# Kernel tuning notes

Hardware: AMD Instinct MI355X
Metric: run time of the kernel (lower is better)

Reference implementation:

```python
import jax, jax.numpy as jnp
import numpy as np

N_NODES = 20000
IN_CH = 128
OUT_CH = 128
HEADS = 1
OB_DIM = 4
N_STEP = 32           # = HEADS*OUT_CH*8 // 32
D_PE = 16             # 32 - HEADS*16
N_EDGES = 256000


def setup_inputs() -> dict:
    key = jax.random.key(0)
    ks = jax.random.split(key, 9)
    x = jax.random.normal(ks[0], (N_NODES, IN_CH), jnp.float32)
    p_t = jax.random.normal(ks[1], (N_STEP, D_PE), jnp.float32)
    edge_index = jax.random.randint(ks[2], (2, N_EDGES), 0, N_NODES, jnp.int32)
    edge_weights = jax.random.uniform(ks[3], (N_EDGES,), jnp.float32)
    # Linear params (PyTorch default init: U(-1/sqrt(fan_in), 1/sqrt(fan_in)))
    s = 1.0 / np.sqrt(IN_CH)
    lin_value_w = jax.random.uniform(ks[4], (IN_CH, HEADS * OUT_CH), jnp.float32, -s, s)
    lin_value_b = jax.random.uniform(ks[5], (HEADS * OUT_CH,), jnp.float32, -s, s)
    inc_w = jax.random.uniform(ks[6], (IN_CH, HEADS * OUT_CH * 8), jnp.float32, -s, s)
    inc_b = jax.random.uniform(ks[7], (HEADS * OUT_CH * 8,), jnp.float32, -s, s)
    g = np.sqrt(6.0 / (N_NODES + HEADS * 16))  # glorot
    map_weights = jax.random.uniform(ks[8], (N_NODES, HEADS * 16), jnp.float32, -g, g)
    return {"x": x, "p_t": p_t, "edge_index": edge_index, "edge_weights": edge_weights,
            "lin_value_w": lin_value_w, "lin_value_b": lin_value_b,
            "inc_w": inc_w, "inc_b": inc_b, "map_weights": map_weights}


def _segment_softmax(gamma, index, num_segments):
    # PyG-style softmax over edges grouped by destination index, per column
    m = jax.ops.segment_max(gamma, index, num_segments=num_segments)     # [N, D]
    num = jnp.exp(gamma - m[index])
    den = jax.ops.segment_sum(num, index, num_segments=num_segments)    # [N, D]
    return num / den[index]


def reference(x, p_t, edge_index, edge_weights, lin_value_w, lin_value_b,
              inc_w, inc_b, map_weights):
    src = edge_index[0]   # x_j side
    dst = edge_index[1]   # x_i side (flow source_to_target)
    n_step = p_t.shape[0]
    E = src.shape[0]

    x_i = x[dst]                                             # [E, in]
    # h_W = increase_dim(x_i).view(E, n_step, 32)
    h_W = (x_i @ inc_w + inc_b).reshape(E, n_step, 32)       # [E, T, 32]
    w_v = map_weights[dst]                                   # [E, 16]
    # beta = mean(h_W * cat([w_v, p_t], -1), -1) computed without materializing aa
    beta = (jnp.einsum('etk,ek->et', h_W[:, :, :16], w_v)
            + jnp.einsum('etk,tk->et', h_W[:, :, 16:], p_t)) / 32.0   # [E, T]

    gamma = beta * edge_weights[:, None]                     # [E, T]
    gamma = jnp.repeat(gamma, OB_DIM, axis=-1)               # [E, T*ob_dim] = [E, H*out]
    all_edge_weights = jnp.mean(gamma, axis=1)               # [E]

    K = int(E * 0.5)
    _, top_idx = jax.lax.top_k(all_edge_weights, K)          # top-K edges
    gamma = gamma[top_idx]                                   # [K, H*out]
    x_i = x_i[top_idx]                                       # [K, in]
    # NOTE: the module re-points aggregation index to edge_index[0] (source)
    index = src[top_idx]                                     # [K]

    gamma = _segment_softmax(gamma, index, N_NODES)          # [K, H*out]

    v = jax.nn.relu(x_i @ lin_value_w + lin_value_b)         # [K, H*out]
    msg = (v.reshape(K, HEADS, OUT_CH)
           * gamma.reshape(K, HEADS, OUT_CH))                # [K, H, out]

    out = jax.ops.segment_sum(msg.reshape(K, HEADS * OUT_CH), index,
                              num_segments=N_NODES)          # scatter-add
    return out                                               # [N, H*out]
```

## Files before the change

kernel.cpp:

```cpp
#include <hip/hip_runtime.h>

#define NN 20000
#define IC 128
#define OC 128
#define NSTEP 32
#define NE 256000
#define KSEL 128000
#define NB 79
#define CH 64
#define ECH 4000
#define RND 16
#define HPW 10000
#define CANDCAP 65536
#define NQCOL 704

struct SelState {
  unsigned long long prefix;
  unsigned r;
  unsigned selc;
  unsigned tiec;
  unsigned done[8];
};

typedef __attribute__((ext_vector_type(16))) float f16v;

__global__ void k_init(const float* __restrict__ p_t, const float* __restrict__ lin_w,
                       const float* __restrict__ lin_b,
                       const float* __restrict__ inc_w, const float* __restrict__ inc_b,
                       float* __restrict__ Wq,
                       double* __restrict__ Ud, double* __restrict__ ubd,
                       unsigned* __restrict__ hist, SelState* st) {
  int i = blockIdx.x * blockDim.x + threadIdx.x;
  if (i < 33 * NQCOL) {
    int k4 = i / NQCOL, col = i - k4 * NQCOL;
    float4 o;
    float* ov = (float*)&o;
    for (int jj = 0; jj < 4; ++jj) {
      int k = 4 * k4 + jj;
      float v = 0.f;
      if (col < 512) {
        int t = col >> 4, c = col & 15;
        if (k < 128) v = inc_w[k * 1024 + t * 32 + c];
        else if (k == 128) v = inc_b[t * 32 + c];
      } else if (col < 544) {
        int t = col - 512;
        if (k < 128) {
          float a = 0.f;
          for (int q = 0; q < 16; ++q) a += inc_w[k * 1024 + t * 32 + 16 + q] * p_t[t * 16 + q];
          v = a;
        } else if (k == 128) {
          float a = 0.f;
          for (int q = 0; q < 16; ++q) a += inc_b[t * 32 + 16 + q] * p_t[t * 16 + q];
          v = a;
        }
      } else if (col < 672) {
        int c = col - 544;
        if (k < 128) v = lin_w[k * OC + c];
        else if (k == 128) v = lin_b[c];
      }
      ov[jj] = v;
    }
    ((float4*)Wq)[i] = o;
    return;
  }
  i -= 33 * NQCOL;
  if (i < 17 * IC) {
    int c = i >> 7, k = i & 127;
    double a = 0.0;
    if (c < 16) {
      for (int t = 0; t < NSTEP; ++t) a += (double)inc_w[k * 1024 + t * 32 + c];
    } else {
      for (int t = 0; t < NSTEP; ++t)
        for (int q = 0; q < 16; ++q)
          a += (double)inc_w[k * 1024 + t * 32 + 16 + q] * (double)p_t[t * 16 + q];
    }
    Ud[c * IC + k] = a;
    return;
  }
  i -= 17 * IC;
  if (i < 17) {
    double a = 0.0;
    if (i < 16) {
      for (int t = 0; t < NSTEP; ++t) a += (double)inc_b[t * 32 + i];
    } else {
      for (int t = 0; t < NSTEP; ++t)
        for (int q = 0; q < 16; ++q)
          a += (double)inc_b[t * 32 + 16 + q] * (double)p_t[t * 16 + q];
    }
    ubd[i] = a;
    return;
  }
  i -= 17;
  if (i < 512) { hist[i] = 0u; return; }
  i -= 512;
  if (i == 0) {
    st->prefix = 0ull; st->r = KSEL; st->selc = 0u; st->tiec = 0u;
    for (int p = 0; p < 8; ++p) st->done[p] = 0u;
  }
}

#define FMA4(WV, BASE)                                                                        \
  acc[BASE+0] = fmaf(xf.x, WV[0],  fmaf(xf.y, WV[1],  fmaf(xf.z, WV[2],  fmaf(xf.w, WV[3],  acc[BASE+0])))); \
  acc[BASE+1] = fmaf(xf.x, WV[4],  fmaf(xf.y, WV[5],  fmaf(xf.z, WV[6],  fmaf(xf.w, WV[7],  acc[BASE+1])))); \
  acc[BASE+2] = fmaf(xf.x, WV[8],  fmaf(xf.y, WV[9],  fmaf(xf.z, WV[10], fmaf(xf.w, WV[11], acc[BASE+2])))); \
  acc[BASE+3] = fmaf(xf.x, WV[12], fmaf(xf.y, WV[13], fmaf(xf.z, WV[14], fmaf(xf.w, WV[15], acc[BASE+3]))));

__global__ __launch_bounds__(256) void k_node(
    const float* __restrict__ x, const float* __restrict__ mw,
    const float* __restrict__ Wq,
    float* __restrict__ beta, float* __restrict__ V) {
  __shared__ float4 xl[64 * 32];
  int tid = threadIdx.x;
  int g = blockIdx.x;
  int s = blockIdx.y;
  int n0 = g * 64;
  int nvalid = NN - n0; if (nvalid > 64) nvalid = 64;

  for (int i = tid; i < 64 * 32; i += 256) {
    int mm = i >> 5, k4 = i & 31;
    float4 v = make_float4(0.f, 0.f, 0.f, 0.f);
    if (mm < nvalid) v = ((const float4*)(x + (size_t)(n0 + mm) * IC))[k4];
    xl[(mm << 5) + ((k4 + mm) & 31)] = v;
  }
  int m = tid & 63;
  int j = __builtin_amdgcn_readfirstlane(threadIdx.x >> 6);
  __syncthreads();

  for (int r = 0; r < 2; ++r) {
    int u = s * 8 + j + r * 4;
    if (u < 32) {
      float mwr[16];
      {
        int mm = (m < nvalid) ? m : 0;
        const float4* mp = (const float4*)(mw + (size_t)(n0 + mm) * 16);
#pragma unroll
        for (int i = 0; i < 4; ++i) {
          float4 t4 = mp[i];
          mwr[4 * i] = t4.x; mwr[4 * i + 1] = t4.y; mwr[4 * i + 2] = t4.z; mwr[4 * i + 3] = t4.w;
        }
      }
      const f16v*   wb = (const f16v*)Wq + (u << 2);
      const float4* wp = (const float4*)Wq + (512 + u);
      float acc[16], accp;
      {
        const f16v* wkb = wb + 32 * 176;
        f16v b0 = wkb[0], b1 = wkb[1], b2 = wkb[2], b3 = wkb[3];
#pragma unroll
        for (int c = 0; c < 4; ++c) {
          acc[c] = b0[4 * c]; acc[4 + c] = b1[4 * c];
          acc[8 + c] = b2[4 * c]; acc[12 + c] = b3[4 * c];
        }
        accp = wp[32 * NQCOL].x;
      }
      f16v w0 = wb[0], w1 = wb[1], w2 = wb[2], w3 = wb[3];
      float4 pw = wp[0];
      for (int k4 = 0; k4 < 32; ++k4) {
        f16v nw0, nw1, nw2, nw3; float4 npw;
        if (k4 < 31) {
          const f16v* wn = wb + (k4 + 1) * 176;
          nw0 = wn[0]; nw1 = wn[1]; nw2 = wn[2]; nw3 = wn[3];
          npw = wp[(k4 + 1) * NQCOL];
        }
        float4 xf = xl[(m << 5) + ((k4 + m) & 31)];
        FMA4(w0, 0) FMA4(w1, 4) FMA4(w2, 8) FMA4(w3, 12)
        accp = fmaf(xf.x, pw.x, fmaf(xf.y, pw.y, fmaf(xf.z, pw.z, fmaf(xf.w, pw.w, accp))));
        if (k4 < 31) { w0 = nw0; w1 = nw1; w2 = nw2; w3 = nw3; pw = npw; }
      }
      float bs = accp;
#pragma unroll
      for (int c = 0; c < 16; ++c) bs = fmaf(acc[c], mwr[c], bs);
      if (m < nvalid) beta[(size_t)(n0 + m) * NSTEP + u] = bs * (1.f / 32.f);
    } else {
      int vg = u - 32;
      int vc0 = vg << 4;
      const f16v* wb = (const f16v*)Wq + 136 + (vg << 2);
      float acc[16];
      {
        const f16v* wkb = wb + 32 * 176;
        f16v b0 = wkb[0], b1 = wkb[1], b2 = wkb[2], b3 = wkb[3];
#pragma unroll
        for (int c = 0; c < 4; ++c) {
          acc[c] = b0[4 * c]; acc[4 + c] = b1[4 * c];
          acc[8 + c] = b2[4 * c]; acc[12 + c] = b3[4 * c];
        }
      }
      f16v w0 = wb[0], w1 = wb[1], w2 = wb[2], w3 = wb[3];
      for (int k4 = 0; k4 < 32; ++k4) {
        f16v nw0, nw1, nw2, nw3;
        if (k4 < 31) {
          const f16v* wn = wb + (k4 + 1) * 176;
          nw0 = wn[0]; nw1 = wn[1]; nw2 = wn[2]; nw3 = wn[3];
        }
        float4 xf = xl[(m << 5) + ((k4 + m) & 31)];
        FMA4(w0, 0) FMA4(w1, 4) FMA4(w2, 8) FMA4(w3, 12)
        if (k4 < 31) { w0 = nw0; w1 = nw1; w2 = nw2; w3 = nw3; }
      }
      if (m < nvalid) {
        float* vout = V + (size_t)(n0 + m) * OC + vc0;
#pragma unroll
        for (int q = 0; q < 4; ++q) {
          float4 o;
          o.x = fmaxf(acc[4 * q], 0.f);     o.y = fmaxf(acc[4 * q + 1], 0.f);
          o.z = fmaxf(acc[4 * q + 2], 0.f); o.w = fmaxf(acc[4 * q + 3], 0.f);
          ((float4*)vout)[q] = o;
        }
      }
    }
  }
}

__global__ __launch_bounds__(256) void k_s64(
    const float* __restrict__ x, const float* __restrict__ mw,
    const double* __restrict__ Ud, const double* __restrict__ ubd,
    double* __restrict__ s64) {
  __shared__ double udl[17 * 130];
  __shared__ float4 xs[16 * 32];
  int tid = threadIdx.x;
  for (int i = tid; i < 17 * IC; i += 256) {
    int cc = i >> 7, kk = i & 127;
    udl[cc * 130 + kk] = Ud[i];
  }
  int n0 = blockIdx.x * 16;
  for (int i = tid; i < 16 * 32; i += 256) {
    int mm = i >> 5, k4 = i & 31;
    int n = n0 + mm;
    xs[i] = (n < NN) ? ((const float4*)(x + (size_t)n * IC))[k4]
                     : make_float4(0.f, 0.f, 0.f, 0.f);
  }
  __syncthreads();
  int m = tid >> 4, c = tid & 15;
  int n = n0 + m;
  const double* uc  = udl + c * 130;
  const double* u16 = udl + 16 * 130;
  double a = 0.0, a16 = 0.0;
  for (int k4 = 0; k4 < 32; ++k4) {
    float4 xv = xs[(m << 5) + k4];
    a = fma((double)xv.x, uc[4 * k4],     a);
    a = fma((double)xv.y, uc[4 * k4 + 1], a);
    a = fma((double)xv.z, uc[4 * k4 + 2], a);
    a = fma((double)xv.w, uc[4 * k4 + 3], a);
  }
#pragma unroll
  for (int q = 0; q < 2; ++q) {
    int k4 = 2 * c + q;
    float4 xv = xs[(m << 5) + k4];
    a16 = fma((double)xv.x, u16[4 * k4],     a16);
    a16 = fma((double)xv.y, u16[4 * k4 + 1], a16);
    a16 = fma((double)xv.z, u16[4 * k4 + 2], a16);
    a16 = fma((double)xv.w, u16[4 * k4 + 3], a16);
  }
  int nm = (n < NN) ? n : 0;
  double part = (a + ubd[c]) * (double)mw[(size_t)nm * 16 + c] + a16;
#pragma unroll
  for (int d = 1; d < 16; d <<= 1) part += __shfl_xor(part, d, 64);
  if (c == 0 && n < NN) s64[n] = (part + ubd[16]) * (1.0 / 1024.0);
}

__global__ void k_keysel(const int* __restrict__ ei, const float* __restrict__ ew,
                         const double* __restrict__ s64,
                         unsigned long long* __restrict__ keys,
                         unsigned* __restrict__ hist, SelState* st) {
  __shared__ unsigned h[256], suf[256];
  __shared__ int last;
  int tid = threadIdx.x;
  h[tid] = 0u;
  if (tid == 0) last = 0;
  __syncthreads();
  for (int e = blockIdx.x * 256 + tid; e < NE; e += gridDim.x * 256) {
    int d = ei[NE + e];
    double v = s64[d] * (double)ew[e];
    unsigned long long u = (unsigned long long)__double_as_longlong(v);
    u = (u & 0x8000000000000000ull) ? ~u : (u | 0x8000000000000000ull);
    keys[e] = u;
    atomicAdd(&h[(unsigned)(u >> 56)], 1u);
  }
  __syncthreads();
  if (h[tid]) atomicAdd(&hist[tid], h[tid]);
  __threadfence();
  __syncthreads();
  if (tid == 0) {
    if (atomicAdd(&st->done[0], 1u) == gridDim.x - 1) last = 1;
  }
  __syncthreads();
  if (!last) return;
  unsigned c = atomicAdd(&hist[tid], 0u);
  suf[tid] = c;
  __syncthreads();
  for (int d = 1; d < 256; d <<= 1) {
    unsigned v = (tid + d < 256) ? suf[tid + d] : 0u;
    __syncthreads();
    suf[tid] += v;
    __syncthreads();
  }
  unsigned r = st->r;
  unsigned exc = suf[tid] - c;
  if (exc < r && exc + c >= r) {
    st->prefix = (unsigned long long)tid;
    st->r = r - exc;
  }
}

__global__ void k_radix1(const unsigned long long* __restrict__ keys,
                         unsigned* __restrict__ hist, SelState* st) {
  __shared__ unsigned h[256], suf[256];
  __shared__ int last;
  int tid = threadIdx.x;
  h[tid] = 0u;
  if (tid == 0) last = 0;
  unsigned long long pref = st->prefix;
  __syncthreads();
  unsigned* hp = hist + 256;
  for (int e = blockIdx.x * 256 + tid; e < NE; e += gridDim.x * 256) {
    unsigned long long k = keys[e];
    if ((k >> 56) == pref)
      atomicAdd(&h[(unsigned)((k >> 48) & 255ull)], 1u);
  }
  __syncthreads();
  if (h[tid]) atomicAdd(&hp[tid], h[tid]);
  __threadfence();
  __syncthreads();
  if (tid == 0) {
    if (atomicAdd(&st->done[1], 1u) == gridDim.x - 1) last = 1;
  }
  __syncthreads();
  if (!last) return;
  unsigned c = atomicAdd(&hp[tid], 0u);
  suf[tid] = c;
  __syncthreads();
  for (int d = 1; d < 256; d <<= 1) {
    unsigned v = (tid + d < 256) ? suf[tid + d] : 0u;
    __syncthreads();
    suf[tid] += v;
    __syncthreads();
  }
  unsigned r = st->r;
  unsigned exc = suf[tid] - c;
  if (exc < r && exc + c >= r) {
    st->prefix = (st->prefix << 8) | (unsigned long long)tid;
    st->r = r - exc;
  }
}

__global__ void k_candsel(const unsigned long long* __restrict__ keys,
                          SelState* st,
                          unsigned long long* __restrict__ flags,
                          unsigned long long* __restrict__ candk, int* __restrict__ cande) {
  __shared__ unsigned h[256], suf[256];
  __shared__ unsigned long long spref;
  __shared__ unsigned sr;
  __shared__ int last;
  int tid = threadIdx.x;
  if (tid == 0) last = 0;
  unsigned P16 = (unsigned)st->prefix;
  for (int e = blockIdx.x * 256 + tid; e < NE; e += gridDim.x * 256) {
    unsigned long long k = keys[e];
    unsigned t16 = (unsigned)(k >> 48);
    unsigned long long bal = __ballot(t16 > P16);
    if ((tid & 63) == 0) flags[e >> 6] = bal;
    if (t16 == P16) {
      unsigned pos = atomicAdd(&st->tiec, 1u);
      if (pos < CANDCAP) { candk[pos] = k; cande[pos] = e; }
    }
  }
  __threadfence();
  __syncthreads();
  if (tid == 0) {
    if (atomicAdd(&st->done[2], 1u) == gridDim.x - 1) last = 1;
  }
  __syncthreads();
  if (!last) return;
  unsigned C = atomicAdd(&st->tiec, 0u); if (C > CANDCAP) C = CANDCAP;
  if (tid == 0) { spref = (unsigned long long)P16; sr = st->r; }
  __syncthreads();
  for (int p = 2; p < 8; ++p) {
    h[tid] = 0u;
    __syncthreads();
    int shift = 56 - 8 * p;
    unsigned long long pf = spref;
    unsigned r = sr;
    for (unsigned i = tid; i < C; i += 256) {
      unsigned long long k = candk[i];
      if ((k >> (shift + 8)) == pf) atomicAdd(&h[(unsigned)((k >> shift) & 255ull)], 1u);
    }
    __syncthreads();
    suf[tid] = h[tid];
    __syncthreads();
    for (int d = 1; d < 256; d <<= 1) {
      unsigned v = (tid + d < 256) ? suf[tid + d] : 0u;
      __syncthreads();
      suf[tid] += v;
      __syncthreads();
    }
    unsigned exc = suf[tid] - h[tid];
    if (exc < r && exc + h[tid] >= r) {
      spref = (pf << 8) | (unsigned long long)tid;
      sr = r - exc;
    }
    __syncthreads();
  }
  unsigned long long T = spref;
  unsigned needed = sr;
  for (unsigned i = tid; i < C; i += 256) {
    unsigned long long k = candk[i];
    int e2 = cande[i];
    bool take = false;
    if (k > T) take = true;
    else if (k == T) {
      unsigned rank = 0;
      for (unsigned q = 0; q < C; ++q)
        rank += (candk[q] == T && cande[q] < e2) ? 1u : 0u;
      take = (rank < needed);
    }
    if (take) atomicOr(&flags[e2 >> 6], 1ull << (e2 & 63));
  }
}

__global__ __launch_bounds__(256) void k_count1(const int* __restrict__ ei,
                                                const unsigned long long* __restrict__ flags,
                                                unsigned* __restrict__ hpart) {
  __shared__ unsigned hp[HPW];
  int tid = threadIdx.x;
  for (int i = tid; i < HPW; i += 256) hp[i] = 0u;
  __syncthreads();
  int base = blockIdx.x * ECH;
  int lim = base + ECH; if (lim > NE) lim = NE;
  for (int k0 = 0; k0 < RND; k0 += 4) {
    int nn[4]; bool tk[4];
#pragma unroll
    for (int q = 0; q < 4; ++q) {
      int e = base + tid + (k0 + q) * 256;
      bool valid = e < lim;
      unsigned long long w = valid ? flags[e >> 6] : 0ull;
      nn[q] = valid ? ei[e] : 0;
      tk[q] = valid && ((w >> (e & 63)) & 1ull);
    }
#pragma unroll
    for (int q = 0; q < 4; ++q)
      if (tk[q]) atomicAdd(&hp[nn[q] >> 1], 1u << ((nn[q] & 1) * 16));
  }
  __syncthreads();
  unsigned* dst = hpart + (size_t)blockIdx.x * HPW;
  for (int i = tid; i < HPW; i += 256) dst[i] = hp[i];
}

__global__ void k_prefA(const unsigned* __restrict__ hpart,
                        unsigned short* __restrict__ hoffl,
                        unsigned* __restrict__ cnt, unsigned* __restrict__ bsum,
                        unsigned* __restrict__ bbase, unsigned* __restrict__ offar,
                        SelState* st) {
  __shared__ unsigned sd[256];
  __shared__ int last;
  int tid = threadIdx.x;
  if (tid == 0) last = 0;
  int n = blockIdx.x * 256 + tid;
  unsigned tot = 0u;
  if (n < NN) {
    int half = (n & 1) * 16;
    int wi = n >> 1;
#pragma unroll 4
    for (int b = 0; b < CH; ++b) {
      hoffl[(size_t)b * NN + n] = (unsigned short)tot;
      tot += (hpart[(size_t)b * HPW + wi] >> half) & 0xFFFFu;
    }
    cnt[n] = tot;
  }
  sd[tid] = (n < NN) ? tot : 0u;
  __syncthreads();
  for (int s = 128; s > 0; s >>= 1) {
    if (tid < s) sd[tid] += sd[tid + s];
    __syncthreads();
  }
  if (tid == 0) bsum[blockIdx.x] = sd[0];
  __threadfence();
  __syncthreads();
  if (tid == 0) {
    if (atomicAdd(&st->done[3], 1u) == gridDim.x - 1) last = 1;
  }
  __syncthreads();
  if (!last) return;
  unsigned v = (tid < NB) ? bsum[tid] : 0u;
  sd[tid] = v;
  __syncthreads();
  for (int d = 1; d < 256; d <<= 1) {
    unsigned u = (tid >= d) ? sd[tid - d] : 0u;
    __syncthreads();
    sd[tid] += u;
    __syncthreads();
  }
  if (tid < NB) bbase[tid] = sd[tid] - v;
  if (tid == NB - 1) offar[NN] = sd[tid];
}

__global__ void k_prefB(const unsigned* __restrict__ cnt, const unsigned* __restrict__ bbase,
                        unsigned* __restrict__ offar) {
  __shared__ unsigned sd[256];
  int tid = threadIdx.x;
  int n = blockIdx.x * 256 + tid;
  unsigned v = (n < NN) ? cnt[n] : 0u;
  sd[tid] = v;
  __syncthreads();
  for (int d = 1; d < 256; d <<= 1) {
    unsigned u = (tid >= d) ? sd[tid - d] : 0u;
    __syncthreads();
    sd[tid] += u;
    __syncthreads();
  }
  if (n < NN) offar[n] = bbase[blockIdx.x] + sd[tid] - v;
}

__global__ __launch_bounds__(256) void k_scatterC(const int* __restrict__ ei,
                                                  const unsigned long long* __restrict__ flags,
                                                  const unsigned* __restrict__ offar,
                                                  const unsigned short* __restrict__ hoffl,
                                                  int* __restrict__ csr) {
  __shared__ unsigned rel[HPW];
  int tid = threadIdx.x;
  for (int i = tid; i < HPW; i += 256) rel[i] = 0u;
  __syncthreads();
  int base = blockIdx.x * ECH;
  int lim = base + ECH; if (lim > NE) lim = NE;
  const unsigned short* hl = hoffl + (size_t)blockIdx.x * NN;
  for (int k0 = 0; k0 < RND; k0 += 4) {
    int nn[4]; bool tk[4]; unsigned hb4[4];
#pragma unroll
    for (int q = 0; q < 4; ++q) {
      int e = base + tid + (k0 + q) * 256;
      bool valid = e < lim;
      unsigned long long w = valid ? flags[e >> 6] : 0ull;
      tk[q] = valid && ((w >> (e & 63)) & 1ull);
      nn[q] = valid ? ei[e] : 0;
      hb4[q] = tk[q] ? (offar[nn[q]] + (unsigned)hl[nn[q]]) : 0u;
    }
#pragma unroll
    for (int q = 0; q < 4; ++q) {
      if (tk[q]) {
        int half = (nn[q] & 1) * 16;
        unsigned old = atomicAdd(&rel[nn[q] >> 1], 1u << half);
        unsigned r = (old >> half) & 0xFFFFu;
        unsigned pos = hb4[q] + r;
        if (pos < KSEL) csr[pos] = base + tid + (k0 + q) * 256;
      }
    }
  }
}

__global__ __launch_bounds__(128) void k_out(
    const int* __restrict__ ei, const float* __restrict__ ew,
    const float* __restrict__ beta, const float* __restrict__ V,
    const unsigned* __restrict__ offar, const int* __restrict__ csr,
    float* __restrict__ out) {
  __shared__ float B[32][NSTEP];
  __shared__ float m[NSTEP], den[NSTEP], scale[NSTEP];
  __shared__ int dl[32];
  __shared__ float ewl[32];
  int n = blockIdx.x, tid = threadIdx.x;
  unsigned beg = offar[n], end = offar[n + 1];
  if (end > (unsigned)KSEL) end = KSEL;
  if (beg > end) beg = end;
  if (tid < NSTEP) { m[tid] = -INFINITY; den[tid] = 0.f; }
  float acc = 0.f;
  int c = tid, tq = tid >> 2;
  __syncthreads();

  for (unsigned cb = beg; cb < end; cb += 32u) {
    unsigned ce = end - cb; if (ce > 32u) ce = 32u;
    if (tid < (int)ce) {
      int e = csr[cb + tid];
      dl[tid] = ei[NE + e];
      ewl[tid] = ew[e];
    }
    __syncthreads();
    for (int idx = tid; idx < (int)ce * NSTEP; idx += 128) {
      int el = idx >> 5, t = idx & 31;
      B[el][t] = beta[(size_t)dl[el] * NSTEP + t] * ewl[el];
    }
    __syncthreads();
    if (tid < NSTEP) {
      int t = tid;
      float mc = -INFINITY;
      for (int el = 0; el < (int)ce; ++el) mc = fmaxf(mc, B[el][t]);
      float mnew = fmaxf(m[t], mc);
      float sc = expf(m[t] - mnew);
      float s = 0.f;
      for (int el = 0; el < (int)ce; ++el) {
        float g = expf(B[el][t] - mnew);
        B[el][t] = g;
        s += g;
      }
      den[t] = den[t] * sc + s;
      m[t] = mnew;
      scale[t] = sc;
    }
    __syncthreads();
    acc *= scale[tq];
    for (int el = 0; el < (int)ce; ++el)
      acc += V[(size_t)dl[el] * OC + c] * B[el][tq];
    __syncthreads();
  }
  float d = den[tq];
  out[(size_t)n * OC + c] = (d > 0.f) ? acc / d : 0.f;
}

extern "C" void kernel_launch(void* const* d_in, const int* in_sizes, int n_in,
                              void* d_out, int out_size, void* d_ws, size_t ws_size,
                              hipStream_t stream) {
  const float* x     = (const float*)d_in[0];
  const float* p_t   = (const float*)d_in[1];
  const int*   ei    = (const int*)d_in[2];
  const float* ew    = (const float*)d_in[3];
  const float* lin_w = (const float*)d_in[4];
  const float* lin_b = (const float*)d_in[5];
  const float* inc_w = (const float*)d_in[6];
  const float* inc_b = (const float*)d_in[7];
  const float* mw    = (const float*)d_in[8];
  float* out = (float*)d_out;

  char* w = (char*)d_ws;
  size_t off = 0;
  auto alloc = [&](size_t b) -> void* {
    void* p = w + off;
    off += (b + 511) & ~(size_t)511;
    return p;
  };
  float*  Wq    = (float*)alloc((size_t)33 * NQCOL * 4 * 4);
  double* Ud    = (double*)alloc((size_t)17 * IC * 8);
  double* ubd   = (double*)alloc(17 * 8);
  float*  beta  = (float*)alloc((size_t)NN * NSTEP * 4);
  double* s64   = (double*)alloc((size_t)NN * 8);
  float*  V     = (float*)alloc((size_t)NN * OC * 4);
  unsigned long long* keys  = (unsigned long long*)alloc((size_t)NE * 8);
  unsigned long long* flags = (unsigned long long*)alloc((size_t)(NE / 64) * 8);
  unsigned long long* candk = (unsigned long long*)alloc((size_t)CANDCAP * 8);
  int*      cande  = (int*)alloc((size_t)CANDCAP * 4);
  unsigned* hpart  = (unsigned*)alloc((size_t)CH * HPW * 4);
  unsigned short* hoffl = (unsigned short*)alloc((size_t)CH * NN * 2);
  unsigned* cnt    = (unsigned*)alloc((size_t)NN * 4);
  unsigned* offar  = (unsigned*)alloc((size_t)(NN + 1) * 4);
  int*      csr    = (int*)alloc((size_t)KSEL * 4);
  unsigned* hist   = (unsigned*)alloc(512 * 4);
  unsigned* bsum   = (unsigned*)alloc(NB * 4);
  unsigned* bbase  = (unsigned*)alloc(NB * 4);
  SelState* st     = (SelState*)alloc(sizeof(SelState));
  if (off > ws_size) return;

  int init_threads = 33 * NQCOL + 17 * IC + 17 + 512 + 1;
  k_init<<<(init_threads + 255) / 256, 256, 0, stream>>>(p_t, lin_w, lin_b, inc_w, inc_b,
                                                         Wq, Ud, ubd, hist, st);
  k_node<<<dim3((NN + 63) / 64, 5), 256, 0, stream>>>(x, mw, Wq, beta, V);
  k_s64<<<(NN + 15) / 16, 256, 0, stream>>>(x, mw, Ud, ubd, s64);
  k_keysel<<<256, 256, 0, stream>>>(ei, ew, s64, keys, hist, st);
  k_radix1<<<256, 256, 0, stream>>>(keys, hist, st);
  k_candsel<<<256, 256, 0, stream>>>(keys, st, flags, candk, cande);
  k_count1<<<CH, 256, 0, stream>>>(ei, flags, hpart);
  k_prefA<<<NB, 256, 0, stream>>>(hpart, hoffl, cnt, bsum, bbase, offar, st);
  k_prefB<<<NB, 256, 0, stream>>>(cnt, bbase, offar);
  k_scatterC<<<CH, 256, 0, stream>>>(ei, flags, offar, hoffl, csr);
  k_out<<<NN, 128, 0, stream>>>(ei, ew, beta, V, offar, csr, out);
}
```

Measured before the change: 296.0 us.

## Rewrite output aggregation as one wavefront per node with online softmax

The final aggregation kernel now assigns one 64-lane wavefront per destination node, with four nodes per 256-thread block, instead of one 128-thread block per node. Edge indices are loaded per lane and broadcast with shuffles, and each edge is processed through an online softmax that rescales the running max and denominator. This removes the shared-memory staging and the repeated __syncthreads barriers. The cost is a serial per-edge loop with two expf calls and several shuffles per edge, and the two halves of each lane's 32 softmax columns are computed redundantly.

```diff
diff --git a/kernel.cpp b/kernel.cpp
--- a/kernel.cpp
+++ b/kernel.cpp
@@ -544,61 +544,50 @@
   }
 }
 
-__global__ __launch_bounds__(128) void k_out(
+__global__ __launch_bounds__(256) void k_out(
     const int* __restrict__ ei, const float* __restrict__ ew,
     const float* __restrict__ beta, const float* __restrict__ V,
     const unsigned* __restrict__ offar, const int* __restrict__ csr,
     float* __restrict__ out) {
-  __shared__ float B[32][NSTEP];
-  __shared__ float m[NSTEP], den[NSTEP], scale[NSTEP];
-  __shared__ int dl[32];
-  __shared__ float ewl[32];
-  int n = blockIdx.x, tid = threadIdx.x;
+  int n = (blockIdx.x * 256 + threadIdx.x) >> 6;
+  int lane = threadIdx.x & 63;
+  if (n >= NN) return;
   unsigned beg = offar[n], end = offar[n + 1];
   if (end > (unsigned)KSEL) end = KSEL;
   if (beg > end) beg = end;
-  if (tid < NSTEP) { m[tid] = -INFINITY; den[tid] = 0.f; }
-  float acc = 0.f;
-  int c = tid, tq = tid >> 2;
-  __syncthreads();
-
-  for (unsigned cb = beg; cb < end; cb += 32u) {
-    unsigned ce = end - cb; if (ce > 32u) ce = 32u;
-    if (tid < (int)ce) {
-      int e = csr[cb + tid];
-      dl[tid] = ei[NE + e];
-      ewl[tid] = ew[e];
-    }
-    __syncthreads();
-    for (int idx = tid; idx < (int)ce * NSTEP; idx += 128) {
-      int el = idx >> 5, t = idx & 31;
-      B[el][t] = beta[(size_t)dl[el] * NSTEP + t] * ewl[el];
-    }
-    __syncthreads();
-    if (tid < NSTEP) {
-      int t = tid;
-      float mc = -INFINITY;
-      for (int el = 0; el < (int)ce; ++el) mc = fmaxf(mc, B[el][t]);
-      float mnew = fmaxf(m[t], mc);
-      float sc = expf(m[t] - mnew);
-      float s = 0.f;
-      for (int el = 0; el < (int)ce; ++el) {
-        float g = expf(B[el][t] - mnew);
-        B[el][t] = g;
-        s += g;
-      }
-      den[t] = den[t] * sc + s;
-      m[t] = mnew;
-      scale[t] = sc;
-    }
-    __syncthreads();
-    acc *= scale[tq];
-    for (int el = 0; el < (int)ce; ++el)
-      acc += V[(size_t)dl[el] * OC + c] * B[el][tq];
-    __syncthreads();
-  }
-  float d = den[tq];
-  out[(size_t)n * OC + c] = (d > 0.f) ? acc / d : 0.f;
+  float mval = -INFINITY, den = 0.f;
+  float acc0 = 0.f, acc1 = 0.f;
+  int t0 = lane >> 2, t1 = 16 + (lane >> 2);
+  int tl = lane & 31;
+
+  for (unsigned cb = beg; cb < end; cb += 64u) {
+    unsigned ce = end - cb; if (ce > 64u) ce = 64u;
+    int d_l = 0; float w_l = 0.f;
+    if (lane < (int)ce) {
+      int e = csr[cb + lane];
+      d_l = ei[NE + e];
+      w_l = ew[e];
+    }
+    for (int i = 0; i < (int)ce; ++i) {
+      int d = __shfl(d_l, i, 64);
+      float wv = __shfl(w_l, i, 64);
+      float b = beta[(size_t)d * NSTEP + tl] * wv;
+      float mnew = fmaxf(mval, b);
+      float sc = expf(mval - mnew);
+      float gg = expf(b - mnew);
+      den = den * sc + gg;
+      mval = mnew;
+      float sc0 = __shfl(sc, t0, 64), g0 = __shfl(gg, t0, 64);
+      float sc1 = __shfl(sc, t1, 64), g1 = __shfl(gg, t1, 64);
+      const float* vr = V + (size_t)d * OC;
+      acc0 = acc0 * sc0 + vr[lane] * g0;
+      acc1 = acc1 * sc1 + vr[64 + lane] * g1;
+    }
+  }
+  float den0 = __shfl(den, t0, 64);
+  float den1 = __shfl(den, t1, 64);
+  out[(size_t)n * OC + lane]      = (den0 > 0.f) ? acc0 / den0 : 0.f;
+  out[(size_t)n * OC + 64 + lane] = (den1 > 0.f) ? acc1 / den1 : 0.f;
 }
 
 extern "C" void kernel_launch(void* const* d_in, const int* in_sizes, int n_in,
@@ -655,5 +644,5 @@
   k_prefA<<<NB, 256, 0, stream>>>(hpart, hoffl, cnt, bsum, bbase, offar, st);
   k_prefB<<<NB, 256, 0, stream>>>(cnt, bbase, offar);
   k_scatterC<<<CH, 256, 0, stream>>>(ei, flags, offar, hoffl, csr);
-  k_out<<<NN, 128, 0, stream>>>(ei, ew, beta, V, offar, csr, out);
-}
+  k_out<<<(NN * 64 + 255) / 256, 256, 0, stream>>>(ei, ew, beta, V, offar, csr, out);
+}
```

Result: faster. 276.7 us (median of 2 runs) (-6.5%).
